# Optimization experiments

Measured on AMD Instinct MI355X. Metric: run time of the kernel, lower is better.

## Reference

```python
import jax, jax.numpy as jnp
import numpy as np

B, S, UNITS = 32, 4096, 512

def setup_inputs() -> dict:
    key = jax.random.key(0)
    ks = jax.random.split(key, 5)
    scale = 1.0 / np.sqrt(UNITS)
    return {
        "s_prev": jax.random.normal(ks[0], (B, UNITS), dtype=jnp.float32),
        "hidden_states": jax.random.normal(ks[1], (B, S, UNITS), dtype=jnp.float32),
        "Ww": jax.random.normal(ks[2], (UNITS, UNITS), dtype=jnp.float32) * scale,
        "Wb": jnp.zeros((UNITS,), dtype=jnp.float32),
        "Uw": jax.random.normal(ks[3], (UNITS, UNITS), dtype=jnp.float32) * scale,
        "Ub": jnp.zeros((UNITS,), dtype=jnp.float32),
        "Vw": jax.random.normal(ks[4], (UNITS, 1), dtype=jnp.float32) * scale,
        "Vb": jnp.zeros((1,), dtype=jnp.float32),
    }

def reference(s_prev, hidden_states, Ww, Wb, Uw, Ub, Vw, Vb):
    # W(s_prev): [B, 1, U] so it broadcasts over seq axis
    W_s = (s_prev @ Ww + Wb)[:, None, :]
    # U(hidden_states): [B, S, U]
    U_h = jnp.einsum('bsu,uv->bsv', hidden_states, Uw) + Ub
    score = jnp.tanh(W_s + U_h)                      # [B, S, U]
    logits = jnp.einsum('bsu,uo->bso', score, Vw) + Vb  # [B, S, 1]
    weights = jax.nn.softmax(logits, axis=1)         # softmax over seq axis
    context = jnp.sum(weights * hidden_states, axis=1)  # [B, U]
    return (context, weights)
```

## Files before the change

kernel.cpp:

```cpp
#include <hip/hip_runtime.h>
#include <hip/hip_bf16.h>

#define UNITS 512
#define SEQ   4096
#define BATCH 32

typedef __attribute__((ext_vector_type(8))) __bf16 bf16x8;
typedef __attribute__((ext_vector_type(4))) float  f32x4;

__device__ __forceinline__ int swz(int l) { return l ^ (((l >> 6) & 7) << 4); }

__global__ void k_bprep(const float* __restrict__ Uw, __bf16* __restrict__ UwTt) {
    const int c     = blockIdx.x;
    const int half  = blockIdx.y;
    const int kstep = blockIdx.z;
    const int t     = threadIdx.x;
    const int n = half * 256 + t;
    bf16x8 o;
#pragma unroll
    for (int j = 0; j < 8; j++)
        o[j] = (__bf16)Uw[(size_t)(kstep * 32 + c * 8 + j) * UNITS + n];
    const int tile = kstep * 2 + half;
    char* dst = (char*)UwTt + (size_t)tile * 16384 + swz(t * 64 + c * 16);
    *(bf16x8*)dst = o;
}

__global__ void k_wsrow(const float* __restrict__ s_prev, const float* __restrict__ Ww,
                        const float* __restrict__ Wb, const float* __restrict__ Ub,
                        float* __restrict__ ws_Ws) {
    __shared__ float sp[UNITS];
    int b = blockIdx.x, t = threadIdx.x;
    sp[t] = s_prev[b * UNITS + t];
    sp[t + 256] = s_prev[b * UNITS + t + 256];
    __syncthreads();
    float a0 = Wb[t] + Ub[t];
    float a1 = Wb[t + 256] + Ub[t + 256];
#pragma unroll 8
    for (int u = 0; u < UNITS; u++) {
        float s = sp[u];
        a0 += s * Ww[u * UNITS + t];
        a1 += s * Ww[u * UNITS + t + 256];
    }
    ws_Ws[b * UNITS + t] = a0;
    ws_Ws[b * UNITS + t + 256] = a1;
}

#define BM 128
#define BN 256
#define BK 32
#define NSTEP (UNITS / BK)

__launch_bounds__(512, 4)
__global__ void k_logits(const float* __restrict__ hidden, const __bf16* __restrict__ UwTt,
                         const float* __restrict__ wsu, const float* __restrict__ Vw,
                         float* __restrict__ lpart) {
    __shared__ __bf16 Ab[2][BM * BK];
    __shared__ __bf16 Bb[2][BN * BK];
    __shared__ float  lred[BM][4];

    const int t = threadIdx.x;
    const int lane = t & 63, wv = t >> 6;
    const int wm = wv >> 2, wn = wv & 3;
    const int l15 = lane & 15, l4 = lane >> 4;
    const int gx = blockIdx.x;
    const int m0 = blockIdx.y * BM;
    const int b  = m0 >> 12;

    f32x4 acc[4][4];
#pragma unroll
    for (int i = 0; i < 4; i++)
#pragma unroll
        for (int j = 0; j < 4; j++) acc[i][j] = (f32x4){0.f, 0.f, 0.f, 0.f};

    const int sr = t >> 2;
    const int sc = t & 3;
    const float* aRow = hidden + (size_t)(m0 + sr) * UNITS + sc * 8;
    const int aoffW = swz(sr * 64 + sc * 16);

    int aoffR[4], boffR[4];
#pragma unroll
    for (int f = 0; f < 4; f++) {
        aoffR[f] = swz((wm * 64 + f * 16 + l15) * 64 + l4 * 16);
        boffR[f] = swz((wn * 64 + f * 16 + l15) * 64 + l4 * 16);
    }

    auto stageA = [&](int buf, int kk) {
        float4 v0 = *(const float4*)(aRow + kk);
        float4 v1 = *(const float4*)(aRow + kk + 4);
        bf16x8 o;
        o[0] = (__bf16)v0.x; o[1] = (__bf16)v0.y; o[2] = (__bf16)v0.z; o[3] = (__bf16)v0.w;
        o[4] = (__bf16)v1.x; o[5] = (__bf16)v1.y; o[6] = (__bf16)v1.z; o[7] = (__bf16)v1.w;
        *(bf16x8*)((char*)(&Ab[buf][0]) + aoffW) = o;
    };
    auto stageB = [&](int buf, int step) {
        const char* src = (const char*)UwTt + (size_t)(step * 2 + gx) * 16384
                        + wv * 2048 + lane * 16;
        char* dst = (char*)(&Bb[buf][0]) + wv * 2048;
        __builtin_amdgcn_global_load_lds(
            (const __attribute__((address_space(1))) void*)src,
            (__attribute__((address_space(3))) void*)dst, 16, 0, 0);
        __builtin_amdgcn_global_load_lds(
            (const __attribute__((address_space(1))) void*)(src + 1024),
            (__attribute__((address_space(3))) void*)(dst + 1024), 16, 0, 0);
    };

    stageA(0, 0);
    stageB(0, 0);

#pragma unroll 2
    for (int step = 0; step < NSTEP; ++step) {
        __syncthreads();
        const int cur = step & 1;
        if (step + 1 < NSTEP) {
            stageA(cur ^ 1, (step + 1) * BK);
            stageB(cur ^ 1, step + 1);
        }
        bf16x8 a[4], bq[4];
#pragma unroll
        for (int fi = 0; fi < 4; fi++)
            a[fi] = *(const bf16x8*)((char*)(&Ab[cur][0]) + aoffR[fi]);
#pragma unroll
        for (int fj = 0; fj < 4; fj++)
            bq[fj] = *(const bf16x8*)((char*)(&Bb[cur][0]) + boffR[fj]);
#pragma unroll
        for (int fi = 0; fi < 4; fi++)
#pragma unroll
            for (int fj = 0; fj < 4; fj++)
                acc[fi][fj] = __builtin_amdgcn_mfma_f32_16x16x32_bf16(a[fi], bq[fj], acc[fi][fj], 0, 0, 0);
    }

    float wsub[4], vww[4];
#pragma unroll
    for (int fj = 0; fj < 4; fj++) {
        int n = gx * BN + wn * 64 + fj * 16 + l15;
        wsub[fj] = wsu[b * UNITS + n];
        vww[fj]  = Vw[n];
    }
#pragma unroll
    for (int fi = 0; fi < 4; fi++) {
#pragma unroll
        for (int r = 0; r < 4; r++) {
            float p = 0.f;
#pragma unroll
            for (int fj = 0; fj < 4; fj++) {
                float x = acc[fi][fj][r] + wsub[fj];
                float e = __expf(2.f * x);
                p += vww[fj] * (1.f - 2.f / (e + 1.f));
            }
#pragma unroll
            for (int off = 1; off < 16; off <<= 1) p += __shfl_xor(p, off);
            if (l15 == 0) lred[wm * 64 + fi * 16 + l4 * 4 + r][wn] = p;
        }
    }
    __syncthreads();
    if (t < BM) {
        float s = lred[t][0] + lred[t][1] + lred[t][2] + lred[t][3];
        lpart[(size_t)(m0 + t) * 2 + gx] = s;
    }
}

__global__ void k_softmax(const float* __restrict__ lpart, float* __restrict__ wout) {
    __shared__ float ebuf[SEQ];
    __shared__ float red[8];
    int b = blockIdx.x, t = threadIdx.x;
    int lane = t & 63, wv = t >> 6;
    float m = -1e30f;
#pragma unroll
    for (int i = 0; i < 16; i++) {
        int s = t + i * 256;
        size_t idx = ((size_t)b * SEQ + s) * 2;
        float l = lpart[idx] + lpart[idx + 1];
        ebuf[s] = l;
        m = fmaxf(m, l);
    }
#pragma unroll
    for (int off = 32; off >= 1; off >>= 1) m = fmaxf(m, __shfl_xor(m, off));
    if (lane == 0) red[wv] = m;
    __syncthreads();
    m = fmaxf(fmaxf(red[0], red[1]), fmaxf(red[2], red[3]));
    float zs = 0.f;
#pragma unroll
    for (int i = 0; i < 16; i++) {
        int s = t + i * 256;
        float e = __expf(ebuf[s] - m);
        ebuf[s] = e;
        zs += e;
    }
#pragma unroll
    for (int off = 32; off >= 1; off >>= 1) zs += __shfl_xor(zs, off);
    __syncthreads();
    if (lane == 0) red[wv] = zs;
    __syncthreads();
    float inv = 1.f / (red[0] + red[1] + red[2] + red[3]);
#pragma unroll
    for (int i = 0; i < 16; i++) {
        int s = t + i * 256;
        wout[(size_t)b * SEQ + s] = ebuf[s] * inv;
    }
}

__global__ void k_ctxpart(const float* __restrict__ hidden, const float* __restrict__ wout,
                          float* __restrict__ part) {
    int b = blockIdx.y, c = blockIdx.x, t = threadIdx.x;
    const float* w = wout + (size_t)b * SEQ + c * 128;
    const float* h = hidden + ((size_t)b * SEQ + c * 128) * UNITS;
    float2 acc = make_float2(0.f, 0.f);
#pragma unroll 4
    for (int s = 0; s < 128; s++) {
        float ww = w[s];
        float2 v = ((const float2*)(h + (size_t)s * UNITS))[t];
        acc.x += ww * v.x;
        acc.y += ww * v.y;
    }
    ((float2*)(part + ((size_t)(b * 32 + c)) * UNITS))[t] = acc;
}

__global__ void k_ctxreduce(const float* __restrict__ part, float* __restrict__ ctx) {
    int b = blockIdx.x, t = threadIdx.x;
    float s = 0.f;
#pragma unroll
    for (int c = 0; c < 32; c++) s += part[((size_t)(b * 32 + c)) * UNITS + t];
    ctx[(size_t)b * UNITS + t] = s;
}

extern "C" void kernel_launch(void* const* d_in, const int* in_sizes, int n_in,
                              void* d_out, int out_size, void* d_ws, size_t ws_size,
                              hipStream_t stream) {
    const float* s_prev = (const float*)d_in[0];
    const float* hidden = (const float*)d_in[1];
    const float* Ww     = (const float*)d_in[2];
    const float* Wb     = (const float*)d_in[3];
    const float* Uw     = (const float*)d_in[4];
    const float* Ub     = (const float*)d_in[5];
    const float* Vw     = (const float*)d_in[6];

    float* out  = (float*)d_out;
    float* ctx  = out;
    float* wout = out + BATCH * UNITS;

    float* wsf   = (float*)d_ws;
    float* ws_Ws = wsf;
    float* ws_lp = ws_Ws + BATCH * UNITS;
    float* ws_cp = ws_lp + (size_t)BATCH * SEQ * 2;
    __bf16* UwTt = (__bf16*)(ws_cp + (size_t)BATCH * 32 * UNITS);

    k_bprep<<<dim3(4, 2, 16), dim3(256), 0, stream>>>(Uw, UwTt);
    k_wsrow<<<dim3(32), dim3(256), 0, stream>>>(s_prev, Ww, Wb, Ub, ws_Ws);
    k_logits<<<dim3(2, 1024), dim3(512), 0, stream>>>(hidden, UwTt, ws_Ws, Vw, ws_lp);
    k_softmax<<<dim3(32), dim3(256), 0, stream>>>(ws_lp, wout);
    k_ctxpart<<<dim3(32, 32), dim3(256), 0, stream>>>(hidden, wout, ws_cp);
    k_ctxreduce<<<dim3(32), dim3(512), 0, stream>>>(ws_cp, ctx);
}
```

Measured before the change: 209.3 us.

## Deepen k_logits pipeline with register-held A prefetch two steps ahead

Restructures the GEMM main loop so the fp32 hidden-state loads for step s+2 are issued into registers and both LDS buffers are prefetched two steps ahead, with the bf16 convert-and-store to LDS deferred until the step that consumes them. Synchronisation moves to explicit s_waitcnt with vmcnt thresholds plus raw barriers, and s_setprio raises wave priority around the MFMA block. The goal is to hide global-load latency for A better than the prior single-step double buffer, which stalled on the load-convert-store inside each iteration. It costs extra registers for two in-flight float4 pairs and relies on hand-counted vmcnt values, which are fragile if the compiler reorders memory ops.

```diff
diff --git a/kernel.cpp b/kernel.cpp
--- a/kernel.cpp
+++ b/kernel.cpp
@@ -84,15 +84,11 @@
         boffR[f] = swz((wn * 64 + f * 16 + l15) * 64 + l4 * 16);
     }
 
-    auto stageA = [&](int buf, int kk) {
-        float4 v0 = *(const float4*)(aRow + kk);
-        float4 v1 = *(const float4*)(aRow + kk + 4);
-        bf16x8 o;
-        o[0] = (__bf16)v0.x; o[1] = (__bf16)v0.y; o[2] = (__bf16)v0.z; o[3] = (__bf16)v0.w;
-        o[4] = (__bf16)v1.x; o[5] = (__bf16)v1.y; o[6] = (__bf16)v1.z; o[7] = (__bf16)v1.w;
-        *(bf16x8*)((char*)(&Ab[buf][0]) + aoffW) = o;
+    auto issueA = [&](float4& v0, float4& v1, int kk) {
+        v0 = *(const float4*)(aRow + kk);
+        v1 = *(const float4*)(aRow + kk + 4);
     };
-    auto stageB = [&](int buf, int step) {
+    auto issueB = [&](int buf, int step) {
         const char* src = (const char*)UwTt + (size_t)(step * 2 + gx) * 16384
                         + wv * 2048 + lane * 16;
         char* dst = (char*)(&Bb[buf][0]) + wv * 2048;
@@ -104,17 +100,20 @@
             (__attribute__((address_space(3))) void*)(dst + 1024), 16, 0, 0);
     };
 
-    stageA(0, 0);
-    stageB(0, 0);
-
-#pragma unroll 2
-    for (int step = 0; step < NSTEP; ++step) {
-        __syncthreads();
-        const int cur = step & 1;
-        if (step + 1 < NSTEP) {
-            stageA(cur ^ 1, (step + 1) * BK);
-            stageB(cur ^ 1, step + 1);
-        }
+    float4 ev0, ev1, ov0, ov1;
+
+    issueA(ev0, ev1, 0);  issueB(0, 0);
+    issueA(ov0, ov1, BK); issueB(1, 1);
+
+    auto body = [&](int s, int cur, float4& v0, float4& v1, bool last) {
+        bf16x8 o;
+        o[0] = (__bf16)v0.x; o[1] = (__bf16)v0.y; o[2] = (__bf16)v0.z; o[3] = (__bf16)v0.w;
+        o[4] = (__bf16)v1.x; o[5] = (__bf16)v1.y; o[6] = (__bf16)v1.z; o[7] = (__bf16)v1.w;
+        *(bf16x8*)((char*)(&Ab[cur][0]) + aoffW) = o;
+        if (last) asm volatile("s_waitcnt vmcnt(0) lgkmcnt(0)" ::: "memory");
+        else      asm volatile("s_waitcnt vmcnt(4) lgkmcnt(0)" ::: "memory");
+        __builtin_amdgcn_s_barrier();
+
         bf16x8 a[4], bq[4];
 #pragma unroll
         for (int fi = 0; fi < 4; fi++)
@@ -122,12 +121,28 @@
 #pragma unroll
         for (int fj = 0; fj < 4; fj++)
             bq[fj] = *(const bf16x8*)((char*)(&Bb[cur][0]) + boffR[fj]);
+        __builtin_amdgcn_s_setprio(1);
 #pragma unroll
         for (int fi = 0; fi < 4; fi++)
 #pragma unroll
             for (int fj = 0; fj < 4; fj++)
                 acc[fi][fj] = __builtin_amdgcn_mfma_f32_16x16x32_bf16(a[fi], bq[fj], acc[fi][fj], 0, 0, 0);
-    }
+        __builtin_amdgcn_s_setprio(0);
+        asm volatile("s_waitcnt lgkmcnt(0)" ::: "memory");
+        __builtin_amdgcn_s_barrier();
+        __builtin_amdgcn_sched_barrier(0);
+        if (s + 2 < NSTEP) {
+            issueA(v0, v1, (s + 2) * BK);
+            issueB(cur, s + 2);
+        }
+    };
+
+    for (int i = 0; i < 7; i++) {
+        body(2 * i,     0, ev0, ev1, false);
+        body(2 * i + 1, 1, ov0, ov1, false);
+    }
+    body(14, 0, ev0, ev1, false);
+    body(15, 1, ov0, ov1, true);
 
     float wsub[4], vww[4];
 #pragma unroll
```

New measurement: 243.4 us. 1.16x slower.

## Shrink logits GEMM tile to 128x128, defer A conversion, group M tiles for L2 reuse

Applied to the files above, without the earlier changes.

The logits GEMM moves from 128x256 tiles with 512 threads to 128x128 tiles with 256 threads, giving 4096 blocks over four N-quarters. The B pre-pack layout and the partial-logit buffer are reshaped to match. Global loads of the next A tile are now issued before the MFMAs, and the bf16 conversion and LDS store happen after them, so load latency overlaps compute. Blocks are remapped so the four N-quarters of each group of eight M tiles run close together, to reuse hidden-state rows in L2. The cost is that each hidden row is now read by four blocks instead of two, which doubles A loads and the fp32-to-bf16 conversion work.

```diff
diff --git a/kernel.cpp b/kernel.cpp
--- a/kernel.cpp
+++ b/kernel.cpp
@@ -8,21 +8,30 @@
 typedef __attribute__((ext_vector_type(8))) __bf16 bf16x8;
 typedef __attribute__((ext_vector_type(4))) float  f32x4;
 
-__device__ __forceinline__ int swz(int l) { return l ^ (((l >> 6) & 7) << 4); }
+__device__ __forceinline__ int swzB(int l) { return l ^ (((l >> 6) & 7) << 4); }
+
+#define MFMA(A, B, C) __builtin_amdgcn_mfma_f32_16x16x32_bf16(A, B, C, 0, 0, 0)
+#define GLL(SRC, DST) __builtin_amdgcn_global_load_lds( \
+    (const __attribute__((address_space(1))) void*)(SRC), \
+    (__attribute__((address_space(3))) void*)(DST), 16, 0, 0)
 
 __global__ void k_bprep(const float* __restrict__ Uw, __bf16* __restrict__ UwTt) {
-    const int c     = blockIdx.x;
-    const int half  = blockIdx.y;
-    const int kstep = blockIdx.z;
+    const int kstep = blockIdx.x;
+    const int q     = blockIdx.y;
     const int t     = threadIdx.x;
-    const int n = half * 256 + t;
-    bf16x8 o;
-#pragma unroll
-    for (int j = 0; j < 8; j++)
-        o[j] = (__bf16)Uw[(size_t)(kstep * 32 + c * 8 + j) * UNITS + n];
-    const int tile = kstep * 2 + half;
-    char* dst = (char*)UwTt + (size_t)tile * 16384 + swz(t * 64 + c * 16);
-    *(bf16x8*)dst = o;
+    const int nl    = t & 127;
+    const int h     = t >> 7;
+    const int n     = q * 128 + nl;
+    const int k0    = kstep * 32 + h * 16;
+    bf16x8 o0, o1;
+#pragma unroll
+    for (int j = 0; j < 8; j++) {
+        o0[j] = (__bf16)Uw[(size_t)(k0 + j) * UNITS + n];
+        o1[j] = (__bf16)Uw[(size_t)(k0 + 8 + j) * UNITS + n];
+    }
+    char* base = (char*)UwTt + (size_t)(kstep * 4 + q) * 8192;
+    *(bf16x8*)(base + swzB(nl * 64 + h * 32))      = o0;
+    *(bf16x8*)(base + swzB(nl * 64 + h * 32 + 16)) = o1;
 }
 
 __global__ void k_wsrow(const float* __restrict__ s_prev, const float* __restrict__ Ww,
@@ -46,24 +55,27 @@
 }
 
 #define BM 128
-#define BN 256
+#define BN 128
 #define BK 32
 #define NSTEP (UNITS / BK)
 
-__launch_bounds__(512, 4)
+__launch_bounds__(256, 4)
 __global__ void k_logits(const float* __restrict__ hidden, const __bf16* __restrict__ UwTt,
                          const float* __restrict__ wsu, const float* __restrict__ Vw,
                          float* __restrict__ lpart) {
     __shared__ __bf16 Ab[2][BM * BK];
     __shared__ __bf16 Bb[2][BN * BK];
-    __shared__ float  lred[BM][4];
+    __shared__ float  lred[BM][2];
 
     const int t = threadIdx.x;
     const int lane = t & 63, wv = t >> 6;
-    const int wm = wv >> 2, wn = wv & 3;
+    const int wm = wv >> 1, wn = wv & 1;
     const int l15 = lane & 15, l4 = lane >> 4;
-    const int gx = blockIdx.x;
-    const int m0 = blockIdx.y * BM;
+
+    const int id = blockIdx.x;
+    const int gx = (id >> 3) & 3;
+    const int mt = ((id >> 5) << 3) | (id & 7);
+    const int m0 = mt * BM;
     const int b  = m0 >> 12;
 
     f32x4 acc[4][4];
@@ -72,61 +84,76 @@
 #pragma unroll
         for (int j = 0; j < 4; j++) acc[i][j] = (f32x4){0.f, 0.f, 0.f, 0.f};
 
-    const int sr = t >> 2;
-    const int sc = t & 3;
-    const float* aRow = hidden + (size_t)(m0 + sr) * UNITS + sc * 8;
-    const int aoffW = swz(sr * 64 + sc * 16);
+    const int sr = t >> 1;
+    const int sh = t & 1;
+    const float* aRow = hidden + (size_t)(m0 + sr) * UNITS + sh * 16;
+    const int aw0 = swzB(sr * 64 + sh * 32);
+    const int aw1 = swzB(sr * 64 + sh * 32 + 16);
 
     int aoffR[4], boffR[4];
 #pragma unroll
     for (int f = 0; f < 4; f++) {
-        aoffR[f] = swz((wm * 64 + f * 16 + l15) * 64 + l4 * 16);
-        boffR[f] = swz((wn * 64 + f * 16 + l15) * 64 + l4 * 16);
-    }
-
-    auto stageA = [&](int buf, int kk) {
-        float4 v0 = *(const float4*)(aRow + kk);
-        float4 v1 = *(const float4*)(aRow + kk + 4);
-        bf16x8 o;
-        o[0] = (__bf16)v0.x; o[1] = (__bf16)v0.y; o[2] = (__bf16)v0.z; o[3] = (__bf16)v0.w;
-        o[4] = (__bf16)v1.x; o[5] = (__bf16)v1.y; o[6] = (__bf16)v1.z; o[7] = (__bf16)v1.w;
-        *(bf16x8*)((char*)(&Ab[buf][0]) + aoffW) = o;
-    };
-    auto stageB = [&](int buf, int step) {
-        const char* src = (const char*)UwTt + (size_t)(step * 2 + gx) * 16384
-                        + wv * 2048 + lane * 16;
-        char* dst = (char*)(&Bb[buf][0]) + wv * 2048;
-        __builtin_amdgcn_global_load_lds(
-            (const __attribute__((address_space(1))) void*)src,
-            (__attribute__((address_space(3))) void*)dst, 16, 0, 0);
-        __builtin_amdgcn_global_load_lds(
-            (const __attribute__((address_space(1))) void*)(src + 1024),
-            (__attribute__((address_space(3))) void*)(dst + 1024), 16, 0, 0);
-    };
-
-    stageA(0, 0);
-    stageB(0, 0);
+        aoffR[f] = swzB((wm * 64 + f * 16 + l15) * 64 + l4 * 16);
+        boffR[f] = swzB((wn * 64 + f * 16 + l15) * 64 + l4 * 16);
+    }
+
+    const char* bglBase = (const char*)UwTt + (size_t)gx * 8192 + wv * 2048 + lane * 16;
+
+    {
+        float4 v0 = *(const float4*)(aRow);
+        float4 v1 = *(const float4*)(aRow + 4);
+        float4 v2 = *(const float4*)(aRow + 8);
+        float4 v3 = *(const float4*)(aRow + 12);
+        GLL(bglBase,        (char*)Bb[0] + wv * 2048);
+        GLL(bglBase + 1024, (char*)Bb[0] + wv * 2048 + 1024);
+        bf16x8 o0, o1;
+        o0[0]=(__bf16)v0.x; o0[1]=(__bf16)v0.y; o0[2]=(__bf16)v0.z; o0[3]=(__bf16)v0.w;
+        o0[4]=(__bf16)v1.x; o0[5]=(__bf16)v1.y; o0[6]=(__bf16)v1.z; o0[7]=(__bf16)v1.w;
+        o1[0]=(__bf16)v2.x; o1[1]=(__bf16)v2.y; o1[2]=(__bf16)v2.z; o1[3]=(__bf16)v2.w;
+        o1[4]=(__bf16)v3.x; o1[5]=(__bf16)v3.y; o1[6]=(__bf16)v3.z; o1[7]=(__bf16)v3.w;
+        *(bf16x8*)((char*)Ab[0] + aw0) = o0;
+        *(bf16x8*)((char*)Ab[0] + aw1) = o1;
+    }
 
 #pragma unroll 2
-    for (int step = 0; step < NSTEP; ++step) {
+    for (int s = 0; s < NSTEP; ++s) {
+        const int cur = s & 1;
         __syncthreads();
-        const int cur = step & 1;
-        if (step + 1 < NSTEP) {
-            stageA(cur ^ 1, (step + 1) * BK);
-            stageB(cur ^ 1, step + 1);
+
+        float4 v0, v1, v2, v3;
+        if (s + 1 < NSTEP) {
+            v0 = *(const float4*)(aRow + (s + 1) * BK);
+            v1 = *(const float4*)(aRow + (s + 1) * BK + 4);
+            v2 = *(const float4*)(aRow + (s + 1) * BK + 8);
+            v3 = *(const float4*)(aRow + (s + 1) * BK + 12);
+            GLL(bglBase + (size_t)((s + 1) * 4) * 8192,
+                (char*)Bb[cur ^ 1] + wv * 2048);
+            GLL(bglBase + (size_t)((s + 1) * 4) * 8192 + 1024,
+                (char*)Bb[cur ^ 1] + wv * 2048 + 1024);
         }
+
         bf16x8 a[4], bq[4];
 #pragma unroll
         for (int fi = 0; fi < 4; fi++)
-            a[fi] = *(const bf16x8*)((char*)(&Ab[cur][0]) + aoffR[fi]);
+            a[fi] = *(const bf16x8*)((const char*)Ab[cur] + aoffR[fi]);
 #pragma unroll
         for (int fj = 0; fj < 4; fj++)
-            bq[fj] = *(const bf16x8*)((char*)(&Bb[cur][0]) + boffR[fj]);
+            bq[fj] = *(const bf16x8*)((const char*)Bb[cur] + boffR[fj]);
 #pragma unroll
         for (int fi = 0; fi < 4; fi++)
 #pragma unroll
             for (int fj = 0; fj < 4; fj++)
-                acc[fi][fj] = __builtin_amdgcn_mfma_f32_16x16x32_bf16(a[fi], bq[fj], acc[fi][fj], 0, 0, 0);
+                acc[fi][fj] = MFMA(a[fi], bq[fj], acc[fi][fj]);
+
+        if (s + 1 < NSTEP) {
+            bf16x8 o0, o1;
+            o0[0]=(__bf16)v0.x; o0[1]=(__bf16)v0.y; o0[2]=(__bf16)v0.z; o0[3]=(__bf16)v0.w;
+            o0[4]=(__bf16)v1.x; o0[5]=(__bf16)v1.y; o0[6]=(__bf16)v1.z; o0[7]=(__bf16)v1.w;
+            o1[0]=(__bf16)v2.x; o1[1]=(__bf16)v2.y; o1[2]=(__bf16)v2.z; o1[3]=(__bf16)v2.w;
+            o1[4]=(__bf16)v3.x; o1[5]=(__bf16)v3.y; o1[6]=(__bf16)v3.z; o1[7]=(__bf16)v3.w;
+            *(bf16x8*)((char*)Ab[cur ^ 1] + aw0) = o0;
+            *(bf16x8*)((char*)Ab[cur ^ 1] + aw1) = o1;
+        }
     }
 
     float wsub[4], vww[4];
@@ -154,8 +181,7 @@
     }
     __syncthreads();
     if (t < BM) {
-        float s = lred[t][0] + lred[t][1] + lred[t][2] + lred[t][3];
-        lpart[(size_t)(m0 + t) * 2 + gx] = s;
+        lpart[(size_t)(m0 + t) * 4 + gx] = lred[t][0] + lred[t][1];
     }
 }
 
@@ -168,8 +194,8 @@
 #pragma unroll
     for (int i = 0; i < 16; i++) {
         int s = t + i * 256;
-        size_t idx = ((size_t)b * SEQ + s) * 2;
-        float l = lpart[idx] + lpart[idx + 1];
+        size_t idx = ((size_t)b * SEQ + s) * 4;
+        float l = (lpart[idx] + lpart[idx + 1]) + (lpart[idx + 2] + lpart[idx + 3]);
         ebuf[s] = l;
         m = fmaxf(m, l);
     }
@@ -241,12 +267,12 @@
     float* wsf   = (float*)d_ws;
     float* ws_Ws = wsf;
     float* ws_lp = ws_Ws + BATCH * UNITS;
-    float* ws_cp = ws_lp + (size_t)BATCH * SEQ * 2;
+    float* ws_cp = ws_lp + (size_t)BATCH * SEQ * 4;
     __bf16* UwTt = (__bf16*)(ws_cp + (size_t)BATCH * 32 * UNITS);
 
-    k_bprep<<<dim3(4, 2, 16), dim3(256), 0, stream>>>(Uw, UwTt);
+    k_bprep<<<dim3(16, 4), dim3(256), 0, stream>>>(Uw, UwTt);
     k_wsrow<<<dim3(32), dim3(256), 0, stream>>>(s_prev, Ww, Wb, Ub, ws_Ws);
-    k_logits<<<dim3(2, 1024), dim3(512), 0, stream>>>(hidden, UwTt, ws_Ws, Vw, ws_lp);
+    k_logits<<<dim3(4096), dim3(256), 0, stream>>>(hidden, UwTt, ws_Ws, Vw, ws_lp);
     k_softmax<<<dim3(32), dim3(256), 0, stream>>>(ws_lp, wout);
     k_ctxpart<<<dim3(32, 32), dim3(256), 0, stream>>>(hidden, wout, ws_cp);
     k_ctxreduce<<<dim3(32), dim3(512), 0, stream>>>(ws_cp, ctx);
```

Result: slower. 224.4 us (+7.2%).
